# Kernel tuning notes

Measured on AMD Instinct MI355X. Metric: run time of the kernel, lower is better.

The kernel has to match this reference:

```python
import jax, jax.numpy as jnp
import numpy as np

N, E, D_IN, D_OUT = 50000, 800000, 128, 128


def setup_inputs() -> dict:
    key = jax.random.key(0)
    ks = jax.random.split(key, 16)
    # edges with no self-loops (add_remaining_self_loops then simply appends one loop per node)
    row = jax.random.randint(ks[0], (E,), 0, N, dtype=jnp.int32)
    off = jax.random.randint(ks[1], (E,), 1, N, dtype=jnp.int32)
    col = (row + off) % N
    edge_index = jnp.stack([row, col], axis=0)
    s_in = 1.0 / np.sqrt(D_IN)
    s_out = 1.0 / np.sqrt(D_OUT)
    u = lambda k, shape, s: jax.random.uniform(k, shape, jnp.float32, -s, s)
    return {
        "x": jax.random.normal(ks[2], (N, D_IN), jnp.float32),
        "edge_index": edge_index,
        "W_hp": u(ks[3], (D_OUT, D_IN), s_in), "b_hp": u(ks[4], (D_OUT,), s_in),
        "W_lp": u(ks[5], (D_OUT, D_IN), s_in), "b_lp": u(ks[6], (D_OUT,), s_in),
        "W_i": u(ks[7], (D_OUT, D_IN), s_in), "b_i": u(ks[8], (D_OUT,), s_in),
        "wlin_h": u(ks[9], (D_OUT,), s_out), "blin_h": u(ks[10], (), s_out),
        "wlin_l": u(ks[11], (D_OUT,), s_out), "blin_l": u(ks[12], (), s_out),
        "wlin_i": u(ks[13], (D_OUT,), s_out), "blin_i": u(ks[14], (), s_out),
    }


def reference(x, edge_index, W_hp, b_hp, W_lp, b_lp, W_i, b_i,
              wlin_h, blin_h, wlin_l, blin_l, wlin_i, blin_i):
    n = x.shape[0]
    row, col = edge_index[0], edge_index[1]
    loop = jnp.arange(n, dtype=row.dtype)
    rf = jnp.concatenate([row, loop])  # sources incl. self-loops
    cf = jnp.concatenate([col, loop])  # targets incl. self-loops
    w = jnp.ones(rf.shape[0], x.dtype)
    # symmetric GCN normalization: D^{-1/2} A_hat D^{-1/2}
    deg = jax.ops.segment_sum(w, cf, num_segments=n)
    dinv = jnp.where(deg > 0, deg ** -0.5, 0.0).astype(x.dtype)
    w = dinv[rf] * w * dinv[cf]

    def agg(h):  # out[i] = sum_j w_e * h[j] over edges j->i
        return jax.ops.segment_sum(w[:, None] * h[rf], cf, num_segments=n)

    h_hp = x @ W_hp.T + b_hp
    H_hp = jax.nn.relu(h_hp - agg(h_hp))          # high-pass
    h_lp = x @ W_lp.T + b_lp
    H_lp = jax.nn.relu(agg(h_lp))                 # low-pass
    H_i = jax.nn.relu(x @ W_i.T + b_i)            # identity

    a_h = jax.nn.sigmoid(H_hp @ wlin_h + blin_h)  # [N]
    a_l = jax.nn.sigmoid(H_lp @ wlin_l + blin_l)
    a_i = jax.nn.sigmoid(H_i @ wlin_i + blin_i)
    # diag(alpha) @ H == alpha[:, None] * H
    return a_h[:, None] * H_hp + a_l[:, None] * H_lp + a_i[:, None] * H_i
```

## Files before the change

### kernel.cpp

```cpp
#include <hip/hip_runtime.h>
#include <cstdint>
#include <cstddef>

#define DEV __device__ __forceinline__

typedef __bf16 bf16x8 __attribute__((ext_vector_type(8)));
typedef float f32x4 __attribute__((ext_vector_type(4)));
typedef unsigned short ushort8v __attribute__((ext_vector_type(8)));

DEV ushort f2b(float f) {
  uint u = __float_as_uint(f);
  return (ushort)((u + 0x7FFFu + ((u >> 16) & 1u)) >> 16);
}

DEV float4 shfl_xor4(float4 v, int m) {
  float4 r;
  r.x = __shfl_xor(v.x, m); r.y = __shfl_xor(v.y, m);
  r.z = __shfl_xor(v.z, m); r.w = __shfl_xor(v.w, m);
  return r;
}

DEV float4 unpack4(uint2 u) {
  float4 r;
  r.x = __uint_as_float(u.x << 16);
  r.y = __uint_as_float(u.x & 0xFFFF0000u);
  r.z = __uint_as_float(u.y << 16);
  r.w = __uint_as_float(u.y & 0xFFFF0000u);
  return r;
}

DEV void fma4(float4& a, float w, uint2 u) {
  float4 v = unpack4(u);
  a.x = fmaf(w, v.x, a.x); a.y = fmaf(w, v.y, a.y);
  a.z = fmaf(w, v.z, a.z); a.w = fmaf(w, v.w, a.w);
}

__global__ __launch_bounds__(512) void k_gemm_fused(
    const float* __restrict__ x,
    const float* __restrict__ W0, const float* __restrict__ W1,
    const float* __restrict__ W2,
    const float* __restrict__ b_hp, const float* __restrict__ b_lp,
    const float* __restrict__ b_i,
    ushort* __restrict__ h_all, int* __restrict__ cnt, int N) {
  int tid = (int)threadIdx.x;
  {
    int gsz = (int)gridDim.x * 512;
    for (int i = (int)blockIdx.x * 512 + tid; i < N; i += gsz) cnt[i] = 0;
  }

  __shared__ ushort Wl[16384];
  int lane = tid & 63, wv = tid >> 6;
  int r = lane & 15, g = lane >> 4;
  int NT = N >> 4;
  int t = blockIdx.x * 8 + wv;
  bool active = t < NT;

  bf16x8 Af[4];
  if (active) {
    const float* xp = x + ((size_t)t * 16 + r) * 128 + g * 8;
#pragma unroll
    for (int kc = 0; kc < 4; ++kc) {
      float4 v0 = *(const float4*)(xp + kc * 32);
      float4 v1 = *(const float4*)(xp + kc * 32 + 4);
      ushort8v u;
      u[0] = f2b(v0.x); u[1] = f2b(v0.y); u[2] = f2b(v0.z); u[3] = f2b(v0.w);
      u[4] = f2b(v1.x); u[5] = f2b(v1.y); u[6] = f2b(v1.z); u[7] = f2b(v1.w);
      Af[kc] = __builtin_bit_cast(bf16x8, u);
    }
  }

  for (int m = 0; m < 3; ++m) {
    const float* Wsrc = (m == 0) ? W0 : (m == 1) ? W1 : W2;
    __syncthreads();
    for (int i = tid; i < 2048; i += 512) {
      int byte = i << 4;
      int row = byte >> 8;
      int swz = byte ^ ((row & 7) << 4);
      const float* s = Wsrc + (i << 3);
      float4 v0 = *(const float4*)s;
      float4 v1 = *(const float4*)(s + 4);
      ushort8v u;
      u[0] = f2b(v0.x); u[1] = f2b(v0.y); u[2] = f2b(v0.z); u[3] = f2b(v0.w);
      u[4] = f2b(v1.x); u[5] = f2b(v1.y); u[6] = f2b(v1.z); u[7] = f2b(v1.w);
      *(ushort8v*)((char*)Wl + swz) = u;
    }
    __syncthreads();
    if (!active) continue;
    const float* bias = (m == 0) ? b_hp : (m == 1) ? b_lp : b_i;
    f32x4 acc[8];
#pragma unroll
    for (int ct = 0; ct < 8; ++ct) {
      float bb = bias[ct * 16 + r];
      f32x4 c; c[0] = bb; c[1] = bb; c[2] = bb; c[3] = bb;
      acc[ct] = c;
    }
#pragma unroll
    for (int kc = 0; kc < 4; ++kc)
#pragma unroll
      for (int ct = 0; ct < 8; ++ct) {
        int row = ct * 16 + r;
        int byte = row * 256 + kc * 64 + g * 16;
        int swz = byte ^ ((row & 7) << 4);
        bf16x8 B = *(const bf16x8*)((const char*)Wl + swz);
        acc[ct] = __builtin_amdgcn_mfma_f32_16x16x32_bf16(Af[kc], B, acc[ct], 0, 0, 0);
      }
    ushort* op = h_all + (size_t)(t * 16 + g * 4) * 384 + m * 128 + r;
#pragma unroll
    for (int ct = 0; ct < 8; ++ct)
#pragma unroll
      for (int j = 0; j < 4; ++j) {
        float v = acc[ct][j];
        if (m == 2) v = fmaxf(v, 0.f);
        op[(size_t)j * 384 + ct * 16] = f2b(v);
      }
  }
}

__global__ __launch_bounds__(256) void k_count(const int* __restrict__ col,
                                               int* __restrict__ cnt, int E) {
  int e = blockIdx.x * 256 + threadIdx.x;
  if (e < E) atomicAdd(&cnt[col[e]], 1);
}

__global__ __launch_bounds__(256) void k_scanA(const int* __restrict__ cnt,
                                               int* __restrict__ off,
                                               float* __restrict__ dinv,
                                               int* __restrict__ btot, int N) {
  __shared__ int ws[4];
  int t = threadIdx.x, ln = t & 63, wv = t >> 6;
  int i = blockIdx.x * 256 + t;
  int v = (i < N) ? cnt[i] : 0;
  int inc = v;
#pragma unroll
  for (int o = 1; o < 64; o <<= 1) {
    int u = __shfl_up(inc, o);
    if (ln >= o) inc += u;
  }
  if (ln == 63) ws[wv] = inc;
  __syncthreads();
  if (t == 0) {
    int s = 0;
#pragma unroll
    for (int w = 0; w < 4; ++w) { int tmp = ws[w]; ws[w] = s; s += tmp; }
  }
  __syncthreads();
  int excl = ws[wv] + inc - v;
  if (i < N) {
    off[i] = excl;
    dinv[i] = rsqrtf((float)v + 1.0f);
  }
  if (t == 255) btot[blockIdx.x] = excl + v;
}

__global__ __launch_bounds__(256) void k_scanBC(int* __restrict__ off,
                                                const int* __restrict__ btot,
                                                int* __restrict__ cursor,
                                                int N, int E, int NB) {
  __shared__ int ws[4];
  __shared__ int pre_sh[256];
  int t = threadIdx.x, ln = t & 63, wv = t >> 6;
  int v = (t < NB) ? btot[t] : 0;
  int inc = v;
#pragma unroll
  for (int o = 1; o < 64; o <<= 1) {
    int u = __shfl_up(inc, o);
    if (ln >= o) inc += u;
  }
  if (ln == 63) ws[wv] = inc;
  __syncthreads();
  if (t == 0) {
    int s = 0;
#pragma unroll
    for (int w = 0; w < 4; ++w) { int tmp = ws[w]; ws[w] = s; s += tmp; }
  }
  __syncthreads();
  pre_sh[t] = ws[wv] + inc - v;
  __syncthreads();
  int bpre = pre_sh[blockIdx.x];
  int i = blockIdx.x * 256 + t;
  if (i < N) {
    int o = off[i] + bpre;
    off[i] = o;
    cursor[i] = o;
  }
  if (blockIdx.x == 0 && t == 0) off[N] = E;
}

__global__ __launch_bounds__(256) void k_scatter(const int* __restrict__ ei,
                                                 const float* __restrict__ dinv,
                                                 int* __restrict__ cursor,
                                                 int2* __restrict__ edata, int E) {
  int e = blockIdx.x * 256 + threadIdx.x;
  if (e >= E) return;
  int s = ei[e], d = ei[E + e];
  float w = dinv[s] * dinv[d];
  int p = atomicAdd(&cursor[d], 1);
  int2 v; v.x = s; v.y = __float_as_int(w);
  edata[p] = v;
}

__global__ __launch_bounds__(256) void k_agg_final(
    const ushort* __restrict__ h_all, const float* __restrict__ dinv,
    const int* __restrict__ off, const int2* __restrict__ edata,
    const float* __restrict__ wlh, const float* __restrict__ wll,
    const float* __restrict__ wli,
    const float* __restrict__ pbh, const float* __restrict__ pbl,
    const float* __restrict__ pbi,
    float* __restrict__ out, int N) {
  int wv = __builtin_amdgcn_readfirstlane((int)threadIdx.x >> 6);
  int lane = (int)threadIdx.x & 63;
  int node = blockIdx.x * 4 + wv;
  if (node >= N) return;

  const ushort* hb = h_all + 4 * lane;
  int p0 = off[node], p1 = off[node + 1];

  float4 a0 = {0,0,0,0}, a1 = {0,0,0,0}, a2 = {0,0,0,0}, a3 = {0,0,0,0};
  float4 a4 = {0,0,0,0}, a5 = {0,0,0,0}, a6 = {0,0,0,0}, a7 = {0,0,0,0};
  int p = p0;
  for (; p + 8 <= p1; p += 8) {
    int2 e0 = edata[p],     e1 = edata[p + 1], e2 = edata[p + 2], e3 = edata[p + 3];
    int2 e4 = edata[p + 4], e5 = edata[p + 5], e6 = edata[p + 6], e7 = edata[p + 7];
    uint2 u0 = *(const uint2*)(const void*)(hb + (size_t)e0.x * 384);
    uint2 u1 = *(const uint2*)(const void*)(hb + (size_t)e1.x * 384);
    uint2 u2 = *(const uint2*)(const void*)(hb + (size_t)e2.x * 384);
    uint2 u3 = *(const uint2*)(const void*)(hb + (size_t)e3.x * 384);
    uint2 u4 = *(const uint2*)(const void*)(hb + (size_t)e4.x * 384);
    uint2 u5 = *(const uint2*)(const void*)(hb + (size_t)e5.x * 384);
    uint2 u6 = *(const uint2*)(const void*)(hb + (size_t)e6.x * 384);
    uint2 u7 = *(const uint2*)(const void*)(hb + (size_t)e7.x * 384);
    fma4(a0, __int_as_float(e0.y), u0);
    fma4(a1, __int_as_float(e1.y), u1);
    fma4(a2, __int_as_float(e2.y), u2);
    fma4(a3, __int_as_float(e3.y), u3);
    fma4(a4, __int_as_float(e4.y), u4);
    fma4(a5, __int_as_float(e5.y), u5);
    fma4(a6, __int_as_float(e6.y), u6);
    fma4(a7, __int_as_float(e7.y), u7);
  }
  for (; p < p1; ++p) {
    int2 e = edata[p];
    uint2 u = *(const uint2*)(const void*)(hb + (size_t)e.x * 384);
    fma4(a0, __int_as_float(e.y), u);
  }
  float4 own;
  own.x = ((a0.x + a1.x) + (a2.x + a3.x)) + ((a4.x + a5.x) + (a6.x + a7.x));
  own.y = ((a0.y + a1.y) + (a2.y + a3.y)) + ((a4.y + a5.y) + (a6.y + a7.y));
  own.z = ((a0.z + a1.z) + (a2.z + a3.z)) + ((a4.z + a5.z) + (a6.z + a7.z));
  own.w = ((a0.w + a1.w) + (a2.w + a3.w)) + ((a4.w + a5.w) + (a6.w + a7.w));

  float di = dinv[node], wself = di * di;
  float4 sv = unpack4(*(const uint2*)(const void*)(hb + (size_t)node * 384));
  own.x = fmaf(wself, sv.x, own.x); own.y = fmaf(wself, sv.y, own.y);
  own.z = fmaf(wself, sv.z, own.z); own.w = fmaf(wself, sv.w, own.w);

  float4 oth = shfl_xor4(own, 32);
  float4 svo = shfl_xor4(sv, 32);
  bool hpside = (lane < 32);
  float4 hpSelf, aggHp, aggLp;
  hpSelf.x = hpside ? sv.x : svo.x; hpSelf.y = hpside ? sv.y : svo.y;
  hpSelf.z = hpside ? sv.z : svo.z; hpSelf.w = hpside ? sv.w : svo.w;
  aggHp.x = hpside ? own.x : oth.x; aggHp.y = hpside ? own.y : oth.y;
  aggHp.z = hpside ? own.z : oth.z; aggHp.w = hpside ? own.w : oth.w;
  aggLp.x = hpside ? oth.x : own.x; aggLp.y = hpside ? oth.y : own.y;
  aggLp.z = hpside ? oth.z : own.z; aggLp.w = hpside ? oth.w : own.w;

  float4 Hh, Hl;
  Hh.x = fmaxf(hpSelf.x - aggHp.x, 0.f); Hh.y = fmaxf(hpSelf.y - aggHp.y, 0.f);
  Hh.z = fmaxf(hpSelf.z - aggHp.z, 0.f); Hh.w = fmaxf(hpSelf.w - aggHp.w, 0.f);
  Hl.x = fmaxf(aggLp.x, 0.f); Hl.y = fmaxf(aggLp.y, 0.f);
  Hl.z = fmaxf(aggLp.z, 0.f); Hl.w = fmaxf(aggLp.w, 0.f);

  int c4 = 4 * (lane & 31);
  float4 hi4 = unpack4(*(const uint2*)(const void*)(h_all + (size_t)node * 384 + 256 + c4));
  float4 wh = *(const float4*)(wlh + c4);
  float4 wl = *(const float4*)(wll + c4);
  float4 wi = *(const float4*)(wli + c4);

  float dh = Hh.x * wh.x + Hh.y * wh.y + Hh.z * wh.z + Hh.w * wh.w;
  float dl = Hl.x * wl.x + Hl.y * wl.y + Hl.z * wl.z + Hl.w * wl.w;
  float dd = hi4.x * wi.x + hi4.y * wi.y + hi4.z * wi.z + hi4.w * wi.w;
#pragma unroll
  for (int o = 32; o > 0; o >>= 1) {
    dh += __shfl_xor(dh, o);
    dl += __shfl_xor(dl, o);
    dd += __shfl_xor(dd, o);
  }
  float a_h = 1.f / (1.f + __expf(-(0.5f * dh + pbh[0])));
  float a_l = 1.f / (1.f + __expf(-(0.5f * dl + pbl[0])));
  float a_i = 1.f / (1.f + __expf(-(0.5f * dd + pbi[0])));

  if (hpside) {
    float4 o4;
    o4.x = a_h * Hh.x + a_l * Hl.x + a_i * hi4.x;
    o4.y = a_h * Hh.y + a_l * Hl.y + a_i * hi4.y;
    o4.z = a_h * Hh.z + a_l * Hl.z + a_i * hi4.z;
    o4.w = a_h * Hh.w + a_l * Hl.w + a_i * hi4.w;
    *(float4*)(out + (size_t)node * 128 + c4) = o4;
  }
}

extern "C" void kernel_launch(void* const* d_in, const int* in_sizes, int n_in,
                              void* d_out, int out_size, void* d_ws, size_t ws_size,
                              hipStream_t stream) {
  const float* x     = (const float*)d_in[0];
  const int*   ei    = (const int*)d_in[1];
  const float* W_hp  = (const float*)d_in[2];
  const float* b_hp  = (const float*)d_in[3];
  const float* W_lp  = (const float*)d_in[4];
  const float* b_lp  = (const float*)d_in[5];
  const float* W_i   = (const float*)d_in[6];
  const float* b_i   = (const float*)d_in[7];
  const float* wlh   = (const float*)d_in[8];
  const float* pbh   = (const float*)d_in[9];
  const float* wll   = (const float*)d_in[10];
  const float* pbl   = (const float*)d_in[11];
  const float* wli   = (const float*)d_in[12];
  const float* pbi   = (const float*)d_in[13];
  float* out = (float*)d_out;

  int N = in_sizes[0] / 128;
  int E = in_sizes[1] / 2;
  int NB = (N + 255) / 256;

  ushort* h_all = (ushort*)d_ws;
  int2*   edata = (int2*)(h_all + (size_t)N * 384);
  float*  dinv  = (float*)(edata + E);
  int*    cnt   = (int*)(dinv + N);
  int*    off   = cnt + N;
  int*    cursor= off + N + 1;
  int*    btot  = cursor + N;

  k_gemm_fused<<<(N / 16 + 7) / 8, 512, 0, stream>>>(
      x, W_hp, W_lp, W_i, b_hp, b_lp, b_i, h_all, cnt, N);
  k_count<<<(E + 255) / 256, 256, 0, stream>>>(ei + E, cnt, E);
  k_scanA<<<NB, 256, 0, stream>>>(cnt, off, dinv, btot, N);
  k_scanBC<<<NB, 256, 0, stream>>>(off, btot, cursor, N, E, NB);
  k_scatter<<<(E + 255) / 256, 256, 0, stream>>>(ei, dinv, cursor, edata, E);
  k_agg_final<<<(N + 3) / 4, 256, 0, stream>>>(
      h_all, dinv, off, edata, wlh, wll, wli, pbh, pbl, pbi, out, N);
}
```

Before: 260.8 us.

## Merge edge-degree counting into GEMM launch and factor destination normalization out of aggregation

The edge-count atomics move into the GEMM kernel as extra leading blocks, so counting and the three projections run concurrently in one launch. The count buffer is now zeroed with a memset instead of inside the GEMM. GEMM blocks shrink from 512 to 256 threads, which means each block stages the bf16 weights into shared memory for half as many tiles. The scatter kernel now stores only the source dinv, and the aggregation multiplies the destination dinv once per node instead of once per edge, which drops one gather per edge in the scatter.

```diff
diff --git a/kernel.cpp b/kernel.cpp
--- a/kernel.cpp
+++ b/kernel.cpp
@@ -35,24 +35,30 @@
   a.z = fmaf(w, v.z, a.z); a.w = fmaf(w, v.w, a.w);
 }
 
-__global__ __launch_bounds__(512) void k_gemm_fused(
+__global__ __launch_bounds__(256) void k_gemm_count(
     const float* __restrict__ x,
     const float* __restrict__ W0, const float* __restrict__ W1,
     const float* __restrict__ W2,
     const float* __restrict__ b_hp, const float* __restrict__ b_lp,
     const float* __restrict__ b_i,
-    ushort* __restrict__ h_all, int* __restrict__ cnt, int N) {
+    ushort* __restrict__ h_all, int N,
+    const int* __restrict__ col, int* __restrict__ cnt, int E, int nCB) {
+  __shared__ ushort Wl[16384];
   int tid = (int)threadIdx.x;
-  {
-    int gsz = (int)gridDim.x * 512;
-    for (int i = (int)blockIdx.x * 512 + tid; i < N; i += gsz) cnt[i] = 0;
-  }
-
-  __shared__ ushort Wl[16384];
+  int bx = (int)blockIdx.x;
+
+  if (bx < nCB) {
+    int gsz = nCB * 256;
+    for (int e = bx * 256 + tid; e < E; e += gsz)
+      atomicAdd(&cnt[col[e]], 1);
+    return;
+  }
+  bx -= nCB;
+
   int lane = tid & 63, wv = tid >> 6;
   int r = lane & 15, g = lane >> 4;
   int NT = N >> 4;
-  int t = blockIdx.x * 8 + wv;
+  int t = bx * 4 + wv;
   bool active = t < NT;
 
   bf16x8 Af[4];
@@ -72,7 +78,7 @@
   for (int m = 0; m < 3; ++m) {
     const float* Wsrc = (m == 0) ? W0 : (m == 1) ? W1 : W2;
     __syncthreads();
-    for (int i = tid; i < 2048; i += 512) {
+    for (int i = tid; i < 2048; i += 256) {
       int byte = i << 4;
       int row = byte >> 8;
       int swz = byte ^ ((row & 7) << 4);
@@ -116,12 +122,6 @@
   }
 }
 
-__global__ __launch_bounds__(256) void k_count(const int* __restrict__ col,
-                                               int* __restrict__ cnt, int E) {
-  int e = blockIdx.x * 256 + threadIdx.x;
-  if (e < E) atomicAdd(&cnt[col[e]], 1);
-}
-
 __global__ __launch_bounds__(256) void k_scanA(const int* __restrict__ cnt,
                                                int* __restrict__ off,
                                                float* __restrict__ dinv,
@@ -193,9 +193,9 @@
   int e = blockIdx.x * 256 + threadIdx.x;
   if (e >= E) return;
   int s = ei[e], d = ei[E + e];
-  float w = dinv[s] * dinv[d];
+  float ws = dinv[s];
   int p = atomicAdd(&cursor[d], 1);
-  int2 v; v.x = s; v.y = __float_as_int(w);
+  int2 v; v.x = s; v.y = __float_as_int(ws);
   edata[p] = v;
 }
 
@@ -249,10 +249,10 @@
   own.z = ((a0.z + a1.z) + (a2.z + a3.z)) + ((a4.z + a5.z) + (a6.z + a7.z));
   own.w = ((a0.w + a1.w) + (a2.w + a3.w)) + ((a4.w + a5.w) + (a6.w + a7.w));
 
-  float di = dinv[node], wself = di * di;
+  float di = dinv[node];
   float4 sv = unpack4(*(const uint2*)(const void*)(hb + (size_t)node * 384));
-  own.x = fmaf(wself, sv.x, own.x); own.y = fmaf(wself, sv.y, own.y);
-  own.z = fmaf(wself, sv.z, own.z); own.w = fmaf(wself, sv.w, own.w);
+  own.x = (own.x + di * sv.x) * di; own.y = (own.y + di * sv.y) * di;
+  own.z = (own.z + di * sv.z) * di; own.w = (own.w + di * sv.w) * di;
 
   float4 oth = shfl_xor4(own, 32);
   float4 svo = shfl_xor4(sv, 32);
@@ -331,9 +331,12 @@
   int*    cursor= off + N + 1;
   int*    btot  = cursor + N;
 
-  k_gemm_fused<<<(N / 16 + 7) / 8, 512, 0, stream>>>(
-      x, W_hp, W_lp, W_i, b_hp, b_lp, b_i, h_all, cnt, N);
-  k_count<<<(E + 255) / 256, 256, 0, stream>>>(ei + E, cnt, E);
+  int nGB = (N / 16 + 3) / 4;
+  int nCB = 782;
+
+  hipMemsetAsync(cnt, 0, sizeof(int) * N, stream);
+  k_gemm_count<<<nCB + nGB, 256, 0, stream>>>(
+      x, W_hp, W_lp, W_i, b_hp, b_lp, b_i, h_all, N, ei + E, cnt, E, nCB);
   k_scanA<<<NB, 256, 0, stream>>>(cnt, off, dinv, btot, N);
   k_scanBC<<<NB, 256, 0, stream>>>(off, btot, cursor, N, E, NB);
   k_scatter<<<(E + 255) / 256, 256, 0, stream>>>(ei, dinv, cursor, edata, E);
```

After: 271.0 us. 3.9% more time.
